# Kernel optimization log

Hardware: AMD Instinct MI355X
Metric: run time of the kernel (lower is better)

Reference implementation:

```python
import jax, jax.numpy as jnp
import numpy as np

B, N, K = 4, 1024, 32
C_S, C_Z, C_H, H, PQ, PV = 384, 128, 16, 12, 4, 8
INF, EPS = 1e5, 1e-8
LN_EPS = 1e-5


def _quat_to_rot(q):
    # q: [..., 4] unit quaternions -> [..., 3, 3]
    w, x, y, z = q[..., 0], q[..., 1], q[..., 2], q[..., 3]
    r = jnp.stack([
        1 - 2 * (y * y + z * z), 2 * (x * y - w * z), 2 * (x * z + w * y),
        2 * (x * y + w * z), 1 - 2 * (x * x + z * z), 2 * (y * z - w * x),
        2 * (x * z - w * y), 2 * (y * z + w * x), 1 - 2 * (x * x + y * y),
    ], axis=-1)
    return r.reshape(q.shape[:-1] + (3, 3))


def _layernorm(x, scale, bias):
    m = jnp.mean(x, axis=-1, keepdims=True)
    v = jnp.mean((x - m) ** 2, axis=-1, keepdims=True)
    return (x - m) * jax.lax.rsqrt(v + LN_EPS) * scale + bias


def setup_inputs():
    key = jax.random.key(0)
    ks = jax.random.split(key, 16)
    s = jax.random.normal(ks[0], (B, N, C_S), jnp.float32)
    z = jax.random.normal(ks[1], (B, N, K, C_Z), jnp.float32)
    edge_index = jax.random.randint(ks[2], (B, N, K), 0, N, jnp.int32)
    quat = jax.random.normal(ks[3], (B, N, 4), jnp.float32)
    rot = _quat_to_rot(quat / jnp.linalg.norm(quat, axis=-1, keepdims=True))
    trans = 10.0 * jax.random.normal(ks[4], (B, N, 3), jnp.float32)
    s_mask = jnp.ones((B, N), jnp.float32)
    sc_s, sc_z = C_S ** -0.5, C_Z ** -0.5
    return {
        "s": s, "z": z, "edge_index": edge_index, "rot": rot, "trans": trans,
        "s_mask": s_mask,
        "ln_s_scale": jnp.ones((C_S,), jnp.float32),
        "ln_s_bias": jnp.zeros((C_S,), jnp.float32),
        "ln_z_scale": jnp.ones((C_Z,), jnp.float32),
        "ln_z_bias": jnp.zeros((C_Z,), jnp.float32),
        "w_q": sc_s * jax.random.normal(ks[5], (C_S, H * C_H), jnp.float32),
        "w_k": sc_s * jax.random.normal(ks[6], (C_S, H * C_H), jnp.float32),
        "w_v": sc_s * jax.random.normal(ks[7], (C_S, H * C_H), jnp.float32),
        "w_q_pts": sc_s * jax.random.normal(ks[8], (C_S, H * PQ * 3), jnp.float32),
        "w_kv_pts": sc_s * jax.random.normal(ks[9], (C_S, H * (PQ + PV) * 3), jnp.float32),
        "w_b": sc_z * jax.random.normal(ks[10], (C_Z, H), jnp.float32),
        "w_down_z": sc_z * jax.random.normal(ks[11], (C_Z, C_Z // 4), jnp.float32),
        "head_weights": jnp.full((H,), 0.541324854612918, jnp.float32),  # softplus^-1(1)
        "w_out": (H * 80) ** -0.5 * jax.random.normal(ks[12], (H * (C_Z // 4 + C_H + PV * 4), C_S), jnp.float32),
    }


def reference(s, z, edge_index, rot, trans, s_mask, ln_s_scale, ln_s_bias,
              ln_z_scale, ln_z_bias, w_q, w_k, w_v, w_q_pts, w_kv_pts, w_b,
              w_down_z, head_weights, w_out):
    bidx = jnp.arange(B)[:, None, None]
    s_ln = _layernorm(s, ln_s_scale, ln_s_bias)          # [B,N,C_S]
    z_ln = _layernorm(z, ln_z_scale, ln_z_bias)          # [B,N,K,C_Z]

    q = (s_ln @ w_q).reshape(B, N, H, C_H)
    k = (s_ln @ w_k)[bidx, edge_index].reshape(B, N, K, H, C_H)
    v = (s_ln @ w_v)[bidx, edge_index].reshape(B, N, K, H, C_H)

    # query points in global frame (query residue's rigid)
    q_pts = (s_ln @ w_q_pts).reshape(B, N, H * PQ, 3)
    q_pts = jnp.einsum('bnij,bnpj->bnpi', rot, q_pts) + trans[:, :, None]
    q_pts = q_pts.reshape(B, N, H, PQ, 3)

    # kv points: gather neighbor local points, then (as in source) apply the
    # QUERY residue's rigid r[..., None, None]
    kv = (s_ln @ w_kv_pts)[bidx, edge_index].reshape(B, N, K, H * (PQ + PV), 3)
    kv = jnp.einsum('bnij,bnkpj->bnkpi', rot, kv) + trans[:, :, None, None]
    kv = kv.reshape(B, N, K, H, PQ + PV, 3)
    k_pts, v_pts = kv[..., :PQ, :], kv[..., PQ:, :]

    b_bias = z_ln @ w_b                                   # [B,N,K,H]
    a = jnp.einsum('bnhc,bnkhc->bnkh', q, k) * (1.0 / (3 * C_H)) ** 0.5
    a = a + (1.0 / 3.0) ** 0.5 * b_bias

    disp = q_pts[:, :, None] - k_pts                      # [B,N,K,H,PQ,3]
    sq = jnp.sum(disp * disp, axis=-1)                    # [B,N,K,H,PQ]
    hw = jax.nn.softplus(head_weights) * (1.0 / (3 * (PQ * 9.0 / 2))) ** 0.5
    a = a - 0.5 * jnp.sum(sq * hw[:, None], axis=-1)      # [B,N,K,H]

    m = s_mask[:, :, None] * s_mask[bidx, edge_index]     # [B,N,K]
    a = a + (INF * (m - 1.0))[..., None]

    a = jax.nn.softmax(jnp.swapaxes(a, -1, -2), axis=-1)  # [B,N,H,K]

    o = jnp.einsum('bnhk,bnkhc->bnhc', a, v).reshape(B, N, H * C_H)

    o_pt = jnp.einsum('bnhk,bnkhvc->bnhvc', a, v_pts)     # [B,N,H,PV,3]
    o_pt = jnp.einsum('bnji,bnhvj->bnhvi', rot, o_pt - trans[:, :, None, None])
    dists = jnp.sqrt(jnp.sum(o_pt * o_pt, axis=-1) + EPS).reshape(B, N, H * PV)
    o_pt_flat = o_pt.reshape(B, N, H * PV * 3)

    o_pair = jnp.einsum('bnhk,bnkc->bnhc', a, z_ln @ w_down_z).reshape(B, N, -1)

    out = jnp.concatenate([o, o_pt_flat, dists, o_pair], axis=-1) @ w_out
    return out
```

## Files before the change

kernel.cpp:

```cpp
#include <hip/hip_runtime.h>
#include <hip/hip_bf16.h>

constexpr int Bb = 4, Nn = 1024, Kk = 32;
constexpr int CS = 384, CZ = 128, CH = 16, Hh = 12, PQn = 4, PVn = 8;
constexpr int HC = Hh * CH;
constexpr int NCOLS = 1152;
constexpr int FEAT = 960;
constexpr int NNODE = Bb * Nn;
constexpr int NEDGE = NNODE * Kk;
constexpr int ZOC = 44;

constexpr int O_WNODE = 4;
constexpr int O_WOUT  = O_WNODE + 384 * 1152;
constexpr int O_WZP   = O_WOUT + 960 * 384;
constexpr int O_BVEC  = O_WZP + 128 * 48;
constexpr int O_SLN   = O_BVEC + 48;
constexpr int O_P     = O_SLN + NNODE * CS;
constexpr int O_ZOUT  = O_P + NNODE * NCOLS;
constexpr int O_FEAT  = O_ZOUT + NEDGE * ZOC;
constexpr int O_MR    = O_FEAT;
constexpr int O_TMP   = O_SLN;
constexpr int TOTAL_F = O_FEAT + NNODE * FEAT;

__device__ __forceinline__ float ldf(const float* p, int i) { return p[i]; }
__device__ __forceinline__ float ldf(const __hip_bfloat16* p, int i) { return __bfloat162float(p[i]); }
__device__ __forceinline__ void stf(float* p, int i, float v) { p[i] = v; }
__device__ __forceinline__ void stf(__hip_bfloat16* p, int i, float v) { p[i] = __float2bfloat16(v); }
__device__ __forceinline__ float4 ld4(const float* p, int i) { return *(const float4*)(p + i); }
__device__ __forceinline__ float4 ld4(const __hip_bfloat16* p, int i) {
    ushort4 u = *(const ushort4*)(p + i);
    return make_float4(__uint_as_float((unsigned)u.x << 16),
                       __uint_as_float((unsigned)u.y << 16),
                       __uint_as_float((unsigned)u.z << 16),
                       __uint_as_float((unsigned)u.w << 16));
}

__global__ void k_detect(const unsigned* smask_raw, int* flag) {
    if (threadIdx.x == 0) *flag = (smask_raw[0] == 0x3F803F80u) ? 1 : 0;
}

template <typename T>
__global__ __launch_bounds__(256) void k_wconv(const T* wq, const T* wk, const T* wv,
                                               const T* wqp, const T* wkvp,
                                               const T* wout, float* wsf,
                                               const int* flag, int want) {
    if (*flag != want) return;
    int idx = blockIdx.x * 256 + threadIdx.x;
    if (idx < 384 * 1152) {
        int row = idx / 1152, col = idx - row * 1152;
        float v;
        if      (col < 192) v = ldf(wq,  row * 192 + col);
        else if (col < 384) v = ldf(wk,  row * 192 + col - 192);
        else if (col < 576) v = ldf(wv,  row * 192 + col - 384);
        else if (col < 720) v = ldf(wqp, row * 144 + col - 576);
        else                v = ldf(wkvp, row * 432 + col - 720);
        wsf[O_WNODE + idx] = v;
    } else if (idx < 384 * 1152 + 960 * 384) {
        int u = idx - 384 * 1152;
        wsf[O_WOUT + u] = ldf(wout, u);
    }
}

template <typename T>
__global__ __launch_bounds__(256) void k_wzprep(const T* wb, const T* wdz, const T* zsc, const T* zbi,
                                                float* wzp, float* bvec, const int* flag, int want) {
    if (*flag != want) return;
    int t = threadIdx.x;
    if (t < 128) {
        float sc = ldf(zsc, t);
        for (int o = 0; o < 48; o++) {
            float w = 0.f;
            if (o < 12)      w = ldf(wb, t * 12 + o);
            else if (o < 44) w = ldf(wdz, t * 32 + o - 12);
            wzp[t * 48 + o] = sc * w;
        }
    } else if (t < 128 + 48) {
        int o = t - 128;
        float acc = 0.f;
        if (o < 44)
            for (int c = 0; c < 128; c++)
                acc += ldf(zbi, c) * (o < 12 ? ldf(wb, c * 12 + o) : ldf(wdz, c * 32 + o - 12));
        bvec[o] = acc;
    }
}

template <typename T>
__global__ __launch_bounds__(384) void k_sln(const T* s, const T* sc, const T* bi,
                                             float* sln, const int* flag, int want) {
    if (*flag != want) return;
    int row = blockIdx.x, t = threadIdx.x;
    float x = ldf(s, row * CS + t);
    float sum = x, sq = x * x;
    #pragma unroll
    for (int m = 32; m; m >>= 1) { sum += __shfl_xor(sum, m, 64); sq += __shfl_xor(sq, m, 64); }
    __shared__ float ssum[6], ssq[6];
    int w = t >> 6;
    if ((t & 63) == 0) { ssum[w] = sum; ssq[w] = sq; }
    __syncthreads();
    if (t == 0) {
        float S = 0, Q = 0;
        for (int i = 0; i < 6; i++) { S += ssum[i]; Q += ssq[i]; }
        ssum[0] = S; ssq[0] = Q;
    }
    __syncthreads();
    float mean = ssum[0] * (1.f / CS);
    float var  = ssq[0] * (1.f / CS) - mean * mean;
    float r = rsqrtf(var + 1e-5f);
    sln[row * CS + t] = (x - mean) * r * ldf(sc, t) + ldf(bi, t);
}

template <typename T>
__global__ __launch_bounds__(256) void k_zstats(const T* z, float* mr, const int* flag, int want) {
    if (*flag != want) return;
    int t = threadIdx.x, r = t >> 5, lane = t & 31;
    int row = blockIdx.x * 8 + r;
    float4 v = ld4(z, row * CZ + lane * 4);
    float sum = v.x + v.y + v.z + v.w;
    float sq  = v.x * v.x + v.y * v.y + v.z * v.z + v.w * v.w;
    #pragma unroll
    for (int m = 16; m; m >>= 1) { sum += __shfl_xor(sum, m, 64); sq += __shfl_xor(sq, m, 64); }
    if (lane == 0) {
        float mean = sum * (1.f / CZ);
        float var  = sq * (1.f / CZ) - mean * mean;
        mr[row * 2]     = mean;
        mr[row * 2 + 1] = rsqrtf(var + 1e-5f);
    }
}

template <typename T>
__global__ __launch_bounds__(256) void k_zgemm(const T* z, const float* mr, const float* wzp,
                                               const float* bvec, float* zout,
                                               const int* flag, int want) {
    if (*flag != want) return;
    __shared__ float Ws[128 * 48];
    __shared__ float As[16][260];
    int t = threadIdx.x;
    int edge0 = blockIdx.x * 256;
    for (int i = t; i < 128 * 48; i += 256) Ws[i] = wzp[i];
    int tm = t >> 2, tn = t & 3, col = tn * 12;
    int sr = t >> 2, q = t & 3;
    float mu[4], rs[4];
    #pragma unroll
    for (int u = 0; u < 4; u++) {
        int e = edge0 + sr + 64 * u;
        mu[u] = mr[e * 2]; rs[u] = mr[e * 2 + 1];
    }
    float acc[4][12];
    #pragma unroll
    for (int i = 0; i < 4; i++)
        #pragma unroll
        for (int j = 0; j < 12; j++) acc[i][j] = bvec[col + j];
    for (int kt = 0; kt < CZ; kt += 16) {
        float4 zv[4];
        #pragma unroll
        for (int u = 0; u < 4; u++) zv[u] = ld4(z, (edge0 + sr + 64 * u) * CZ + kt + q * 4);
        __syncthreads();
        #pragma unroll
        for (int u = 0; u < 4; u++) {
            int rr = sr + 64 * u;
            As[q * 4 + 0][rr] = (zv[u].x - mu[u]) * rs[u];
            As[q * 4 + 1][rr] = (zv[u].y - mu[u]) * rs[u];
            As[q * 4 + 2][rr] = (zv[u].z - mu[u]) * rs[u];
            As[q * 4 + 3][rr] = (zv[u].w - mu[u]) * rs[u];
        }
        __syncthreads();
        #pragma unroll
        for (int kk = 0; kk < 16; kk++) {
            float4 a = *(const float4*)&As[kk][tm * 4];
            const float* wr = &Ws[(kt + kk) * 48 + col];
            float4 b0 = *(const float4*)(wr);
            float4 b1 = *(const float4*)(wr + 4);
            float4 b2 = *(const float4*)(wr + 8);
            float av[4]  = {a.x, a.y, a.z, a.w};
            float bv[12] = {b0.x, b0.y, b0.z, b0.w, b1.x, b1.y, b1.z, b1.w, b2.x, b2.y, b2.z, b2.w};
            #pragma unroll
            for (int i = 0; i < 4; i++)
                #pragma unroll
                for (int j = 0; j < 12; j++) acc[i][j] += av[i] * bv[j];
        }
    }
    #pragma unroll
    for (int i = 0; i < 4; i++) {
        int e = edge0 + tm * 4 + i;
        #pragma unroll
        for (int j = 0; j < 12; j++) {
            int c = col + j;
            if (c < ZOC) zout[e * ZOC + c] = acc[i][j];
        }
    }
}

__global__ __launch_bounds__(256) void k_gemm(const float* A, int lda, const float* Bm, int ldb,
                                              float* C, int ldc, int ksplit, int csplit) {
    __shared__ float As[16][68];
    __shared__ float Bs[16][136];
    int t = threadIdx.x;
    int row0 = blockIdx.x * 64, col0 = blockIdx.y * 128;
    int kbeg = blockIdx.z * ksplit, kend = kbeg + ksplit;
    C += (size_t)blockIdx.z * csplit;
    int tx = t & 15, ty = t >> 4;
    int ar = t >> 2, aq = t & 3;
    int bk = t >> 4, bc = (t & 15) * 8;
    float acc[4][8] = {};
    for (int kt = kbeg; kt < kend; kt += 16) {
        float4 a0 = *(const float4*)(A + (row0 + ar) * lda + kt + aq * 4);
        float4 b0 = *(const float4*)(Bm + (kt + bk) * ldb + col0 + bc);
        float4 b1 = *(const float4*)(Bm + (kt + bk) * ldb + col0 + bc + 4);
        __syncthreads();
        As[aq * 4 + 0][ar] = a0.x; As[aq * 4 + 1][ar] = a0.y;
        As[aq * 4 + 2][ar] = a0.z; As[aq * 4 + 3][ar] = a0.w;
        *(float4*)&Bs[bk][bc] = b0;
        *(float4*)&Bs[bk][bc + 4] = b1;
        __syncthreads();
        #pragma unroll
        for (int kk = 0; kk < 16; kk++) {
            float4 av  = *(const float4*)&As[kk][ty * 4];
            float4 blo = *(const float4*)&Bs[kk][tx * 4];
            float4 bhi = *(const float4*)&Bs[kk][64 + tx * 4];
            float aa[4] = {av.x, av.y, av.z, av.w};
            float bb[8] = {blo.x, blo.y, blo.z, blo.w, bhi.x, bhi.y, bhi.z, bhi.w};
            #pragma unroll
            for (int i = 0; i < 4; i++)
                #pragma unroll
                for (int j = 0; j < 8; j++)
                    acc[i][j] += aa[i] * bb[j];
        }
    }
    #pragma unroll
    for (int i = 0; i < 4; i++) {
        float* Cr = C + (size_t)(row0 + ty * 4 + i) * ldc + col0;
        *(float4*)(Cr + tx * 4)      = make_float4(acc[i][0], acc[i][1], acc[i][2], acc[i][3]);
        *(float4*)(Cr + 64 + tx * 4) = make_float4(acc[i][4], acc[i][5], acc[i][6], acc[i][7]);
    }
}

template <typename TO>
__global__ __launch_bounds__(256) void k_outred(const float* tmp, TO* out, const int* flag, int want) {
    if (*flag != want) return;
    int i = (blockIdx.x * 256 + threadIdx.x) * 4;
    float4 a = *(const float4*)(tmp + i);
    float4 b = *(const float4*)(tmp + NNODE * CS + i);
    stf(out, i,     a.x + b.x); stf(out, i + 1, a.y + b.y);
    stf(out, i + 2, a.z + b.z); stf(out, i + 3, a.w + b.w);
}

template <typename T>
__global__ __launch_bounds__(256, 4) void k_attn(const float* P, const float* zout,
                                                 const int* eidx, const T* smask, const T* rot,
                                                 const T* hwq, float* featg, const int* flag, int want) {
    if (*flag != want) return;
    __shared__ float nds[4][1792];
    __shared__ int js[4][32];
    int w = threadIdx.x >> 6, lane = threadIdx.x & 63;
    int node = blockIdx.x * 4 + w;
    int b = node >> 10;
    float* S = nds[w];
    int* J = js[w];
    const float* Pn = P + (size_t)node * NCOLS;
    for (int u = lane; u < 336; u += 64)
        S[u] = (u < 192) ? Pn[u] : Pn[384 + u];
    if (lane < 32) {
        int j = eidx[node * Kk + lane];
        J[lane] = b * Nn + j;
        S[360 + lane] = ldf(smask, node) * ldf(smask, b * Nn + j);
    } else if (lane < 44) {
        int h = lane - 32;
        float x = ldf(hwq, h);
        S[336 + h] = logf(1.f + expf(x)) * 0.13608276348795434f;
    } else if (lane < 53) {
        int u = lane - 44;
        int i = u / 3, jj = u - i * 3;
        float m = 0;
        #pragma unroll
        for (int l = 0; l < 3; l++)
            m += ldf(rot, node * 9 + l * 3 + i) * ldf(rot, node * 9 + l * 3 + jj);
        S[348 + u] = m;
    }
    __builtin_amdgcn_wave_barrier();
    #pragma unroll
    for (int it = 0; it < 6; it++) {
        int u = lane + 64 * it;
        int h = u >> 5, k = u & 31;
        const float* Pj = P + (size_t)J[k] * NCOLS;
        float qk = 0;
        const float4* pk4 = (const float4*)(Pj + 192 + h * 16);
        const float4* qs4 = (const float4*)(S + h * 16);
        #pragma unroll
        for (int c4 = 0; c4 < 4; c4++) {
            float4 pv = pk4[c4], qv = qs4[c4];
            qk += qv.x * pv.x + qv.y * pv.y + qv.z * pv.z + qv.w * pv.w;
        }
        float M00 = S[348], M01 = S[349], M02 = S[350],
              M11 = S[352], M12 = S[353], M22 = S[356];
        const float4* pp4 = (const float4*)(Pj + 720 + h * 36);
        const float4* qp4 = (const float4*)(S + 192 + h * 12);
        float4 A0 = pp4[0], A1 = pp4[1], A2 = pp4[2];
        float4 B0 = qp4[0], B1 = qp4[1], B2 = qp4[2];
        float d[12] = {B0.x - A0.x, B0.y - A0.y, B0.z - A0.z, B0.w - A0.w,
                       B1.x - A1.x, B1.y - A1.y, B1.z - A1.z, B1.w - A1.w,
                       B2.x - A2.x, B2.y - A2.y, B2.z - A2.z, B2.w - A2.w};
        float sq = 0;
        #pragma unroll
        for (int p = 0; p < 4; p++) {
            float d0 = d[p * 3], d1 = d[p * 3 + 1], d2 = d[p * 3 + 2];
            sq += M00 * d0 * d0 + M11 * d1 * d1 + M22 * d2 * d2
                + 2.f * (M01 * d0 * d1 + M02 * d0 * d2 + M12 * d1 * d2);
        }
        float logit = qk * 0.14433756729740643f
                    + 0.5773502691896258f * zout[((size_t)node * Kk + k) * ZOC + h]
                    - 0.5f * S[336 + h] * sq
                    + 1e5f * (S[360 + k] - 1.f);
        float mx = logit;
        #pragma unroll
        for (int m = 16; m; m >>= 1) mx = fmaxf(mx, __shfl_xor(mx, m, 64));
        float e = expf(logit - mx);
        float ssum = e;
        #pragma unroll
        for (int m = 16; m; m >>= 1) ssum += __shfl_xor(ssum, m, 64);
        S[392 + u] = e / ssum;
    }
    __builtin_amdgcn_wave_barrier();
    for (int u = lane; u < 216; u += 64) {
        int h, off, fbase, pair = 0;
        if (u < 48)       { h = u >> 2; off = 384 + h * 16 + (u & 3) * 4; fbase = h * 16 + (u & 3) * 4; }
        else if (u < 120) { int v = u - 48;  h = v / 6; int q = v - h * 6;
                            off = 732 + h * 36 + q * 4; fbase = 192 + h * 24 + q * 4; }
        else              { int v = u - 120; h = v >> 3;
                            off = 12 + (v & 7) * 4; fbase = 576 + h * 32 + (v & 7) * 4; pair = 1; }
        float4 acc = {0.f, 0.f, 0.f, 0.f};
        const float* lrow = S + 392 + h * 32;
        if (!pair) {
            #pragma unroll 8
            for (int k = 0; k < 32; k++) {
                float lw = lrow[k];
                float4 pv = *(const float4*)(P + (size_t)J[k] * NCOLS + off);
                acc.x += lw * pv.x; acc.y += lw * pv.y; acc.z += lw * pv.z; acc.w += lw * pv.w;
            }
        } else {
            const float* zr = zout + (size_t)node * Kk * ZOC + off;
            #pragma unroll 8
            for (int k = 0; k < 32; k++) {
                float lw = lrow[k];
                float4 pv = *(const float4*)(zr + k * ZOC);
                acc.x += lw * pv.x; acc.y += lw * pv.y; acc.z += lw * pv.z; acc.w += lw * pv.w;
            }
        }
        *(float4*)&S[776 + fbase] = acc;
    }
    __builtin_amdgcn_wave_barrier();
    for (int u = lane; u < 96; u += 64) {
        float r0 = S[776 + 192 + u * 3 + 0];
        float r1 = S[776 + 192 + u * 3 + 1];
        float r2 = S[776 + 192 + u * 3 + 2];
        float o0 = S[348] * r0 + S[349] * r1 + S[350] * r2;
        float o1 = S[351] * r0 + S[352] * r1 + S[353] * r2;
        float o2 = S[354] * r0 + S[355] * r1 + S[356] * r2;
        S[776 + 192 + u * 3 + 0] = o0;
        S[776 + 192 + u * 3 + 1] = o1;
        S[776 + 192 + u * 3 + 2] = o2;
        S[776 + 480 + u] = sqrtf(o0 * o0 + o1 * o1 + o2 * o2 + 1e-8f);
    }
    __builtin_amdgcn_wave_barrier();
    float* og = featg + (size_t)node * FEAT;
    for (int u = lane; u < 240; u += 64)
        *(float4*)(og + u * 4) = *(const float4*)&S[776 + u * 4];
}

extern "C" void kernel_launch(void* const* d_in, const int* in_sizes, int n_in,
                              void* d_out, int out_size, void* d_ws, size_t ws_size,
                              hipStream_t stream) {
    float* wsf = (float*)d_ws;
    int* flag = (int*)d_ws;
    const void* s = d_in[0];   const void* z = d_in[1];
    const int* eidx = (const int*)d_in[2];
    const void* rot = d_in[3];
    const void* smask = d_in[5];
    const void* lns_sc = d_in[6]; const void* lns_bi = d_in[7];
    const void* lnz_sc = d_in[8]; const void* lnz_bi = d_in[9];
    const void* wq = d_in[10]; const void* wk = d_in[11]; const void* wv = d_in[12];
    const void* wqp = d_in[13]; const void* wkvp = d_in[14];
    const void* wb = d_in[15]; const void* wdz = d_in[16];
    const void* hwq = d_in[17]; const void* wout = d_in[18];

    k_detect<<<1, 64, 0, stream>>>((const unsigned*)smask, flag);

    constexpr int WCONV_N = (384 * 1152 + 960 * 384) / 256;
    k_wconv<float><<<WCONV_N, 256, 0, stream>>>((const float*)wq, (const float*)wk, (const float*)wv,
        (const float*)wqp, (const float*)wkvp, (const float*)wout, wsf, flag, 0);
    k_wconv<__hip_bfloat16><<<WCONV_N, 256, 0, stream>>>((const __hip_bfloat16*)wq,
        (const __hip_bfloat16*)wk, (const __hip_bfloat16*)wv, (const __hip_bfloat16*)wqp,
        (const __hip_bfloat16*)wkvp, (const __hip_bfloat16*)wout, wsf, flag, 1);

    k_wzprep<float><<<1, 256, 0, stream>>>((const float*)wb, (const float*)wdz,
        (const float*)lnz_sc, (const float*)lnz_bi, wsf + O_WZP, wsf + O_BVEC, flag, 0);
    k_wzprep<__hip_bfloat16><<<1, 256, 0, stream>>>((const __hip_bfloat16*)wb, (const __hip_bfloat16*)wdz,
        (const __hip_bfloat16*)lnz_sc, (const __hip_bfloat16*)lnz_bi, wsf + O_WZP, wsf + O_BVEC, flag, 1);

    k_sln<float><<<NNODE, 384, 0, stream>>>((const float*)s, (const float*)lns_sc, (const float*)lns_bi,
                                            wsf + O_SLN, flag, 0);
    k_sln<__hip_bfloat16><<<NNODE, 384, 0, stream>>>((const __hip_bfloat16*)s, (const __hip_bfloat16*)lns_sc,
                                                     (const __hip_bfloat16*)lns_bi, wsf + O_SLN, flag, 1);

    k_zstats<float><<<NEDGE / 8, 256, 0, stream>>>((const float*)z, wsf + O_MR, flag, 0);
    k_zstats<__hip_bfloat16><<<NEDGE / 8, 256, 0, stream>>>((const __hip_bfloat16*)z, wsf + O_MR, flag, 1);

    k_zgemm<float><<<NEDGE / 256, 256, 0, stream>>>((const float*)z, wsf + O_MR, wsf + O_WZP,
        wsf + O_BVEC, wsf + O_ZOUT, flag, 0);
    k_zgemm<__hip_bfloat16><<<NEDGE / 256, 256, 0, stream>>>((const __hip_bfloat16*)z, wsf + O_MR,
        wsf + O_WZP, wsf + O_BVEC, wsf + O_ZOUT, flag, 1);

    k_gemm<<<dim3(NNODE / 64, NCOLS / 128, 1), 256, 0, stream>>>(
        wsf + O_SLN, CS, wsf + O_WNODE, NCOLS, wsf + O_P, NCOLS, CS, 0);

    k_attn<float><<<NNODE / 4, 256, 0, stream>>>(wsf + O_P, wsf + O_ZOUT, eidx,
        (const float*)smask, (const float*)rot, (const float*)hwq, wsf + O_FEAT, flag, 0);
    k_attn<__hip_bfloat16><<<NNODE / 4, 256, 0, stream>>>(wsf + O_P, wsf + O_ZOUT, eidx,
        (const float*)smask == nullptr ? (const __hip_bfloat16*)smask : (const __hip_bfloat16*)smask,
        (const __hip_bfloat16*)rot, (const __hip_bfloat16*)hwq, wsf + O_FEAT, flag, 1);

    k_gemm<<<dim3(NNODE / 64, CS / 128, 2), 256, 0, stream>>>(
        wsf + O_FEAT, FEAT, wsf + O_WOUT, CS, wsf + O_TMP, CS, FEAT / 2, NNODE * CS);
    k_outred<float><<<NNODE * CS / 1024, 256, 0, stream>>>(wsf + O_TMP, (float*)d_out, flag, 0);
    k_outred<__hip_bfloat16><<<NNODE * CS / 1024, 256, 0, stream>>>(wsf + O_TMP,
        (__hip_bfloat16*)d_out, flag, 1);
}
```

Measured before the change: 389.0 us.

## Fuse prep kernels, fold z layernorm into GEMM epilogue, drop split-K output

Merges weight conversion, s-layernorm and z-weight prep into one launch, and folds the z layernorm statistics into the z GEMM by applying mean and rstd algebraically in the epilogue through a column-sum vector. The split-K output GEMM plus reduction kernel is replaced by a single smaller-tile GEMM that writes the output directly. Host-side dtype detection from input sizes skips the detect kernel and the duplicate dtype-guarded launches. The attention kernel also gets a swizzled block-to-node mapping, a padded softmax row stride and a dropped occupancy hint. Computing variance from E[x^2]-mean^2 on raw z can lose precision, and the output GEMM has less parallelism without split-K.

```diff
diff --git a/kernel.cpp b/kernel.cpp
--- a/kernel.cpp
+++ b/kernel.cpp
@@ -14,12 +14,11 @@
 constexpr int O_WOUT  = O_WNODE + 384 * 1152;
 constexpr int O_WZP   = O_WOUT + 960 * 384;
 constexpr int O_BVEC  = O_WZP + 128 * 48;
-constexpr int O_SLN   = O_BVEC + 48;
+constexpr int O_CSUM  = O_BVEC + 48;
+constexpr int O_SLN   = O_CSUM + 48;
 constexpr int O_P     = O_SLN + NNODE * CS;
 constexpr int O_ZOUT  = O_P + NNODE * NCOLS;
 constexpr int O_FEAT  = O_ZOUT + NEDGE * ZOC;
-constexpr int O_MR    = O_FEAT;
-constexpr int O_TMP   = O_SLN;
 constexpr int TOTAL_F = O_FEAT + NNODE * FEAT;
 
 __device__ __forceinline__ float ldf(const float* p, int i) { return p[i]; }
@@ -40,128 +39,107 @@
 }
 
 template <typename T>
-__global__ __launch_bounds__(256) void k_wconv(const T* wq, const T* wk, const T* wv,
-                                               const T* wqp, const T* wkvp,
-                                               const T* wout, float* wsf,
-                                               const int* flag, int want) {
-    if (*flag != want) return;
-    int idx = blockIdx.x * 256 + threadIdx.x;
-    if (idx < 384 * 1152) {
-        int row = idx / 1152, col = idx - row * 1152;
-        float v;
-        if      (col < 192) v = ldf(wq,  row * 192 + col);
-        else if (col < 384) v = ldf(wk,  row * 192 + col - 192);
-        else if (col < 576) v = ldf(wv,  row * 192 + col - 384);
-        else if (col < 720) v = ldf(wqp, row * 144 + col - 576);
-        else                v = ldf(wkvp, row * 432 + col - 720);
-        wsf[O_WNODE + idx] = v;
-    } else if (idx < 384 * 1152 + 960 * 384) {
-        int u = idx - 384 * 1152;
-        wsf[O_WOUT + u] = ldf(wout, u);
+__global__ __launch_bounds__(384) void k_prep(const T* s, const T* lns_sc, const T* lns_bi,
+                                              const T* wq, const T* wk, const T* wv,
+                                              const T* wqp, const T* wkvp, const T* wout,
+                                              const T* wb, const T* wdz, const T* zsc, const T* zbi,
+                                              float* wsf, const int* flag, int want) {
+    if (flag && *flag != want) return;
+    int blk = blockIdx.x, t = threadIdx.x;
+    __shared__ float ssum[6], ssq[6];
+    if (blk < 2112) {
+        int idx = blk * 384 + t;
+        if (idx < 384 * 1152) {
+            int row = idx / 1152, col = idx - row * 1152;
+            float v;
+            if      (col < 192) v = ldf(wq,  row * 192 + col);
+            else if (col < 384) v = ldf(wk,  row * 192 + col - 192);
+            else if (col < 576) v = ldf(wv,  row * 192 + col - 384);
+            else if (col < 720) v = ldf(wqp, row * 144 + col - 576);
+            else                v = ldf(wkvp, row * 432 + col - 720);
+            wsf[O_WNODE + idx] = v;
+        } else {
+            int u = idx - 384 * 1152;
+            wsf[O_WOUT + u] = ldf(wout, u);
+        }
+    } else if (blk < 2112 + 4096) {
+        int row = blk - 2112;
+        float x = ldf(s, row * CS + t);
+        float sum = x, sq = x * x;
+        #pragma unroll
+        for (int m = 32; m; m >>= 1) { sum += __shfl_xor(sum, m, 64); sq += __shfl_xor(sq, m, 64); }
+        int w = t >> 6;
+        if ((t & 63) == 0) { ssum[w] = sum; ssq[w] = sq; }
+        __syncthreads();
+        if (t == 0) {
+            float S = 0, Q = 0;
+            for (int i = 0; i < 6; i++) { S += ssum[i]; Q += ssq[i]; }
+            ssum[0] = S; ssq[0] = Q;
+        }
+        __syncthreads();
+        float mean = ssum[0] * (1.f / CS);
+        float var  = ssq[0] * (1.f / CS) - mean * mean;
+        float r = rsqrtf(var + 1e-5f);
+        wsf[O_SLN + row * CS + t] = (x - mean) * r * ldf(lns_sc, t) + ldf(lns_bi, t);
+    } else {
+        if (t < 128) {
+            float sc = ldf(zsc, t);
+            for (int o = 0; o < 48; o++) {
+                float w = 0.f;
+                if (o < 12)      w = ldf(wb, t * 12 + o);
+                else if (o < 44) w = ldf(wdz, t * 32 + o - 12);
+                wsf[O_WZP + t * 48 + o] = sc * w;
+            }
+        } else if (t < 176) {
+            int o = t - 128;
+            float acc = 0.f;
+            if (o < 44)
+                for (int c = 0; c < 128; c++)
+                    acc += ldf(zbi, c) * (o < 12 ? ldf(wb, c * 12 + o) : ldf(wdz, c * 32 + o - 12));
+            wsf[O_BVEC + o] = acc;
+        } else if (t < 224) {
+            int o = t - 176;
+            float acc = 0.f;
+            if (o < 44)
+                for (int c = 0; c < 128; c++)
+                    acc += ldf(zsc, c) * (o < 12 ? ldf(wb, c * 12 + o) : ldf(wdz, c * 32 + o - 12));
+            wsf[O_CSUM + o] = acc;
+        }
     }
 }
 
 template <typename T>
-__global__ __launch_bounds__(256) void k_wzprep(const T* wb, const T* wdz, const T* zsc, const T* zbi,
-                                                float* wzp, float* bvec, const int* flag, int want) {
-    if (*flag != want) return;
-    int t = threadIdx.x;
-    if (t < 128) {
-        float sc = ldf(zsc, t);
-        for (int o = 0; o < 48; o++) {
-            float w = 0.f;
-            if (o < 12)      w = ldf(wb, t * 12 + o);
-            else if (o < 44) w = ldf(wdz, t * 32 + o - 12);
-            wzp[t * 48 + o] = sc * w;
-        }
-    } else if (t < 128 + 48) {
-        int o = t - 128;
-        float acc = 0.f;
-        if (o < 44)
-            for (int c = 0; c < 128; c++)
-                acc += ldf(zbi, c) * (o < 12 ? ldf(wb, c * 12 + o) : ldf(wdz, c * 32 + o - 12));
-        bvec[o] = acc;
-    }
-}
-
-template <typename T>
-__global__ __launch_bounds__(384) void k_sln(const T* s, const T* sc, const T* bi,
-                                             float* sln, const int* flag, int want) {
-    if (*flag != want) return;
-    int row = blockIdx.x, t = threadIdx.x;
-    float x = ldf(s, row * CS + t);
-    float sum = x, sq = x * x;
-    #pragma unroll
-    for (int m = 32; m; m >>= 1) { sum += __shfl_xor(sum, m, 64); sq += __shfl_xor(sq, m, 64); }
-    __shared__ float ssum[6], ssq[6];
-    int w = t >> 6;
-    if ((t & 63) == 0) { ssum[w] = sum; ssq[w] = sq; }
-    __syncthreads();
-    if (t == 0) {
-        float S = 0, Q = 0;
-        for (int i = 0; i < 6; i++) { S += ssum[i]; Q += ssq[i]; }
-        ssum[0] = S; ssq[0] = Q;
-    }
-    __syncthreads();
-    float mean = ssum[0] * (1.f / CS);
-    float var  = ssq[0] * (1.f / CS) - mean * mean;
-    float r = rsqrtf(var + 1e-5f);
-    sln[row * CS + t] = (x - mean) * r * ldf(sc, t) + ldf(bi, t);
-}
-
-template <typename T>
-__global__ __launch_bounds__(256) void k_zstats(const T* z, float* mr, const int* flag, int want) {
-    if (*flag != want) return;
-    int t = threadIdx.x, r = t >> 5, lane = t & 31;
-    int row = blockIdx.x * 8 + r;
-    float4 v = ld4(z, row * CZ + lane * 4);
-    float sum = v.x + v.y + v.z + v.w;
-    float sq  = v.x * v.x + v.y * v.y + v.z * v.z + v.w * v.w;
-    #pragma unroll
-    for (int m = 16; m; m >>= 1) { sum += __shfl_xor(sum, m, 64); sq += __shfl_xor(sq, m, 64); }
-    if (lane == 0) {
-        float mean = sum * (1.f / CZ);
-        float var  = sq * (1.f / CZ) - mean * mean;
-        mr[row * 2]     = mean;
-        mr[row * 2 + 1] = rsqrtf(var + 1e-5f);
-    }
-}
-
-template <typename T>
-__global__ __launch_bounds__(256) void k_zgemm(const T* z, const float* mr, const float* wzp,
-                                               const float* bvec, float* zout,
-                                               const int* flag, int want) {
-    if (*flag != want) return;
+__global__ __launch_bounds__(256) void k_zg(const T* z, const float* wzp, const float* bvec,
+                                            const float* csum, float* zout,
+                                            const int* flag, int want) {
+    if (flag && *flag != want) return;
     __shared__ float Ws[128 * 48];
     __shared__ float As[16][260];
+    __shared__ float mus[256], rss[256];
     int t = threadIdx.x;
     int edge0 = blockIdx.x * 256;
     for (int i = t; i < 128 * 48; i += 256) Ws[i] = wzp[i];
     int tm = t >> 2, tn = t & 3, col = tn * 12;
     int sr = t >> 2, q = t & 3;
-    float mu[4], rs[4];
-    #pragma unroll
-    for (int u = 0; u < 4; u++) {
-        int e = edge0 + sr + 64 * u;
-        mu[u] = mr[e * 2]; rs[u] = mr[e * 2 + 1];
-    }
-    float acc[4][12];
-    #pragma unroll
-    for (int i = 0; i < 4; i++)
-        #pragma unroll
-        for (int j = 0; j < 12; j++) acc[i][j] = bvec[col + j];
+    float psum[4] = {}, psq[4] = {};
+    float acc[4][12] = {};
     for (int kt = 0; kt < CZ; kt += 16) {
         float4 zv[4];
         #pragma unroll
-        for (int u = 0; u < 4; u++) zv[u] = ld4(z, (edge0 + sr + 64 * u) * CZ + kt + q * 4);
+        for (int u = 0; u < 4; u++) {
+            zv[u] = ld4(z, (edge0 + sr + 64 * u) * CZ + kt + q * 4);
+            psum[u] += zv[u].x + zv[u].y + zv[u].z + zv[u].w;
+            psq[u]  += zv[u].x * zv[u].x + zv[u].y * zv[u].y
+                     + zv[u].z * zv[u].z + zv[u].w * zv[u].w;
+        }
         __syncthreads();
         #pragma unroll
         for (int u = 0; u < 4; u++) {
             int rr = sr + 64 * u;
-            As[q * 4 + 0][rr] = (zv[u].x - mu[u]) * rs[u];
-            As[q * 4 + 1][rr] = (zv[u].y - mu[u]) * rs[u];
-            As[q * 4 + 2][rr] = (zv[u].z - mu[u]) * rs[u];
-            As[q * 4 + 3][rr] = (zv[u].w - mu[u]) * rs[u];
+            As[q * 4 + 0][rr] = zv[u].x;
+            As[q * 4 + 1][rr] = zv[u].y;
+            As[q * 4 + 2][rr] = zv[u].z;
+            As[q * 4 + 3][rr] = zv[u].w;
         }
         __syncthreads();
         #pragma unroll
@@ -178,34 +156,47 @@
                 #pragma unroll
                 for (int j = 0; j < 12; j++) acc[i][j] += av[i] * bv[j];
         }
-    }
+        __syncthreads();
+    }
+    #pragma unroll
+    for (int u = 0; u < 4; u++) {
+        float s = psum[u], qq = psq[u];
+        s += __shfl_xor(s, 1, 64); s += __shfl_xor(s, 2, 64);
+        qq += __shfl_xor(qq, 1, 64); qq += __shfl_xor(qq, 2, 64);
+        if (q == 0) {
+            float mu = s * (1.f / CZ);
+            mus[sr + 64 * u] = mu;
+            rss[sr + 64 * u] = rsqrtf(qq * (1.f / CZ) - mu * mu + 1e-5f);
+        }
+    }
+    __syncthreads();
     #pragma unroll
     for (int i = 0; i < 4; i++) {
-        int e = edge0 + tm * 4 + i;
+        int r = tm * 4 + i;
+        float mu = mus[r], rs = rss[r];
+        int e = edge0 + r;
         #pragma unroll
         for (int j = 0; j < 12; j++) {
             int c = col + j;
-            if (c < ZOC) zout[e * ZOC + c] = acc[i][j];
+            if (c < ZOC) zout[(size_t)e * ZOC + c] = rs * acc[i][j] - rs * mu * csum[c] + bvec[c];
         }
     }
 }
 
 __global__ __launch_bounds__(256) void k_gemm(const float* A, int lda, const float* Bm, int ldb,
-                                              float* C, int ldc, int ksplit, int csplit) {
+                                              float* C, int ldc, int Kdim) {
     __shared__ float As[16][68];
     __shared__ float Bs[16][136];
     int t = threadIdx.x;
     int row0 = blockIdx.x * 64, col0 = blockIdx.y * 128;
-    int kbeg = blockIdx.z * ksplit, kend = kbeg + ksplit;
-    C += (size_t)blockIdx.z * csplit;
     int tx = t & 15, ty = t >> 4;
     int ar = t >> 2, aq = t & 3;
     int bk = t >> 4, bc = (t & 15) * 8;
     float acc[4][8] = {};
-    for (int kt = kbeg; kt < kend; kt += 16) {
-        float4 a0 = *(const float4*)(A + (row0 + ar) * lda + kt + aq * 4);
-        float4 b0 = *(const float4*)(Bm + (kt + bk) * ldb + col0 + bc);
-        float4 b1 = *(const float4*)(Bm + (kt + bk) * ldb + col0 + bc + 4);
+    for (int kt = 0; kt < Kdim; kt += 16) {
+        float4 a0 = *(const float4*)(A + (size_t)(row0 + ar) * lda + kt + aq * 4);
+        float4 b0 = *(const float4*)(Bm + (size_t)(kt + bk) * ldb + col0 + bc);
+        float4 b1 = *(const float4*)(Bm + (size_t)(kt + bk) * ldb + col0 + bc + 4);
         __syncthreads();
         As[aq * 4 + 0][ar] = a0.x; As[aq * 4 + 1][ar] = a0.y;
         As[aq * 4 + 2][ar] = a0.z; As[aq * 4 + 3][ar] = a0.w;
@@ -235,24 +226,56 @@
 }
 
 template <typename TO>
-__global__ __launch_bounds__(256) void k_outred(const float* tmp, TO* out, const int* flag, int want) {
-    if (*flag != want) return;
-    int i = (blockIdx.x * 256 + threadIdx.x) * 4;
-    float4 a = *(const float4*)(tmp + i);
-    float4 b = *(const float4*)(tmp + NNODE * CS + i);
-    stf(out, i,     a.x + b.x); stf(out, i + 1, a.y + b.y);
-    stf(out, i + 2, a.z + b.z); stf(out, i + 3, a.w + b.w);
+__global__ __launch_bounds__(256) void k_gout(const float* A, const float* Bm, TO* C,
+                                              const int* flag, int want) {
+    if (flag && *flag != want) return;
+    __shared__ float As[16][36];
+    __shared__ float Bs[16][68];
+    int t = threadIdx.x;
+    int row0 = blockIdx.x * 32, col0 = blockIdx.y * 64;
+    int ar = (t >> 2) & 31, aq = t & 3;
+    int bk = t >> 4, bc = (t & 15) * 4;
+    int ty = t >> 4, tx = t & 15;
+    int m0 = ty * 2, n0 = tx * 4;
+    float acc[2][4] = {};
+    for (int kt = 0; kt < FEAT; kt += 16) {
+        float4 av = {};
+        if (t < 128) av = *(const float4*)(A + (size_t)(row0 + ar) * FEAT + kt + aq * 4);
+        float4 bv = *(const float4*)(Bm + (size_t)(kt + bk) * CS + col0 + bc);
+        __syncthreads();
+        if (t < 128) {
+            As[aq * 4 + 0][ar] = av.x; As[aq * 4 + 1][ar] = av.y;
+            As[aq * 4 + 2][ar] = av.z; As[aq * 4 + 3][ar] = av.w;
+        }
+        *(float4*)&Bs[bk][bc] = bv;
+        __syncthreads();
+        #pragma unroll
+        for (int kk = 0; kk < 16; kk++) {
+            float a0 = As[kk][m0], a1 = As[kk][m0 + 1];
+            float4 b = *(const float4*)&Bs[kk][n0];
+            acc[0][0] += a0 * b.x; acc[0][1] += a0 * b.y; acc[0][2] += a0 * b.z; acc[0][3] += a0 * b.w;
+            acc[1][0] += a1 * b.x; acc[1][1] += a1 * b.y; acc[1][2] += a1 * b.z; acc[1][3] += a1 * b.w;
+        }
+        __syncthreads();
+    }
+    #pragma unroll
+    for (int i = 0; i < 2; i++)
+        #pragma unroll
+        for (int j = 0; j < 4; j++)
+            stf(C, (size_t)(row0 + m0 + i) * CS + col0 + n0 + j, acc[i][j]);
 }
 
 template <typename T>
-__global__ __launch_bounds__(256, 4) void k_attn(const float* P, const float* zout,
-                                                 const int* eidx, const T* smask, const T* rot,
-                                                 const T* hwq, float* featg, const int* flag, int want) {
-    if (*flag != want) return;
-    __shared__ float nds[4][1792];
+__global__ __launch_bounds__(256) void k_attn(const float* P, const float* zout,
+                                              const int* eidx, const T* smask, const T* rot,
+                                              const T* hwq, float* featg, const int* flag, int want) {
+    if (flag && *flag != want) return;
+    __shared__ float nds[4][1760];
     __shared__ int js[4][32];
+    int bid = blockIdx.x;
+    int nb = ((bid & 7) << 7) + (bid >> 3);
     int w = threadIdx.x >> 6, lane = threadIdx.x & 63;
-    int node = blockIdx.x * 4 + w;
+    int node = nb * 4 + w;
     int b = node >> 10;
     float* S = nds[w];
     int* J = js[w];
@@ -317,7 +340,7 @@
         float ssum = e;
         #pragma unroll
         for (int m = 16; m; m >>= 1) ssum += __shfl_xor(ssum, m, 64);
-        S[392 + u] = e / ssum;
+        S[392 + h * 33 + k] = e / ssum;
     }
     __builtin_amdgcn_wave_barrier();
     for (int u = lane; u < 216; u += 64) {
@@ -328,7 +351,7 @@
         else              { int v = u - 120; h = v >> 3;
                             off = 12 + (v & 7) * 4; fbase = 576 + h * 32 + (v & 7) * 4; pair = 1; }
         float4 acc = {0.f, 0.f, 0.f, 0.f};
-        const float* lrow = S + 392 + h * 32;
+        const float* lrow = S + 392 + h * 33;
         if (!pair) {
             #pragma unroll 8
             for (int k = 0; k < 32; k++) {
@@ -345,25 +368,25 @@
                 acc.x += lw * pv.x; acc.y += lw * pv.y; acc.z += lw * pv.z; acc.w += lw * pv.w;
             }
         }
-        *(float4*)&S[776 + fbase] = acc;
+        *(float4*)&S[788 + fbase] = acc;
     }
     __builtin_amdgcn_wave_barrier();
     for (int u = lane; u < 96; u += 64) {
-        float r0 = S[776 + 192 + u * 3 + 0];
-        float r1 = S[776 + 192 + u * 3 + 1];
-        float r2 = S[776 + 192 + u * 3 + 2];
+        float r0 = S[788 + 192 + u * 3 + 0];
+        float r1 = S[788 + 192 + u * 3 + 1];
+        float r2 = S[788 + 192 + u * 3 + 2];
         float o0 = S[348] * r0 + S[349] * r1 + S[350] * r2;
         float o1 = S[351] * r0 + S[352] * r1 + S[353] * r2;
         float o2 = S[354] * r0 + S[355] * r1 + S[356] * r2;
-        S[776 + 192 + u * 3 + 0] = o0;
-        S[776 + 192 + u * 3 + 1] = o1;
-        S[776 + 192 + u * 3 + 2] = o2;
-        S[776 + 480 + u] = sqrtf(o0 * o0 + o1 * o1 + o2 * o2 + 1e-8f);
+        S[788 + 192 + u * 3 + 0] = o0;
+        S[788 + 192 + u * 3 + 1] = o1;
+        S[788 + 192 + u * 3 + 2] = o2;
+        S[788 + 480 + u] = sqrtf(o0 * o0 + o1 * o1 + o2 * o2 + 1e-8f);
     }
     __builtin_amdgcn_wave_barrier();
     float* og = featg + (size_t)node * FEAT;
     for (int u = lane; u < 240; u += 64)
-        *(float4*)(og + u * 4) = *(const float4*)&S[776 + u * 4];
+        *(float4*)(og + u * 4) = *(const float4*)&S[788 + u * 4];
 }
 
 extern "C" void kernel_launch(void* const* d_in, const int* in_sizes, int n_in,
@@ -382,45 +405,57 @@
     const void* wb = d_in[15]; const void* wdz = d_in[16];
     const void* hwq = d_in[17]; const void* wout = d_in[18];
 
-    k_detect<<<1, 64, 0, stream>>>((const unsigned*)smask, flag);
-
-    constexpr int WCONV_N = (384 * 1152 + 960 * 384) / 256;
-    k_wconv<float><<<WCONV_N, 256, 0, stream>>>((const float*)wq, (const float*)wk, (const float*)wv,
-        (const float*)wqp, (const float*)wkvp, (const float*)wout, wsf, flag, 0);
-    k_wconv<__hip_bfloat16><<<WCONV_N, 256, 0, stream>>>((const __hip_bfloat16*)wq,
-        (const __hip_bfloat16*)wk, (const __hip_bfloat16*)wv, (const __hip_bfloat16*)wqp,
-        (const __hip_bfloat16*)wkvp, (const __hip_bfloat16*)wout, wsf, flag, 1);
-
-    k_wzprep<float><<<1, 256, 0, stream>>>((const float*)wb, (const float*)wdz,
-        (const float*)lnz_sc, (const float*)lnz_bi, wsf + O_WZP, wsf + O_BVEC, flag, 0);
-    k_wzprep<__hip_bfloat16><<<1, 256, 0, stream>>>((const __hip_bfloat16*)wb, (const __hip_bfloat16*)wdz,
-        (const __hip_bfloat16*)lnz_sc, (const __hip_bfloat16*)lnz_bi, wsf + O_WZP, wsf + O_BVEC, flag, 1);
-
-    k_sln<float><<<NNODE, 384, 0, stream>>>((const float*)s, (const float*)lns_sc, (const float*)lns_bi,
-                                            wsf + O_SLN, flag, 0);
-    k_sln<__hip_bfloat16><<<NNODE, 384, 0, stream>>>((const __hip_bfloat16*)s, (const __hip_bfloat16*)lns_sc,
-                                                     (const __hip_bfloat16*)lns_bi, wsf + O_SLN, flag, 1);
-
-    k_zstats<float><<<NEDGE / 8, 256, 0, stream>>>((const float*)z, wsf + O_MR, flag, 0);
-    k_zstats<__hip_bfloat16><<<NEDGE / 8, 256, 0, stream>>>((const __hip_bfloat16*)z, wsf + O_MR, flag, 1);
-
-    k_zgemm<float><<<NEDGE / 256, 256, 0, stream>>>((const float*)z, wsf + O_MR, wsf + O_WZP,
-        wsf + O_BVEC, wsf + O_ZOUT, flag, 0);
-    k_zgemm<__hip_bfloat16><<<NEDGE / 256, 256, 0, stream>>>((const __hip_bfloat16*)z, wsf + O_MR,
-        wsf + O_WZP, wsf + O_BVEC, wsf + O_ZOUT, flag, 1);
-
-    k_gemm<<<dim3(NNODE / 64, NCOLS / 128, 1), 256, 0, stream>>>(
-        wsf + O_SLN, CS, wsf + O_WNODE, NCOLS, wsf + O_P, NCOLS, CS, 0);
-
-    k_attn<float><<<NNODE / 4, 256, 0, stream>>>(wsf + O_P, wsf + O_ZOUT, eidx,
-        (const float*)smask, (const float*)rot, (const float*)hwq, wsf + O_FEAT, flag, 0);
-    k_attn<__hip_bfloat16><<<NNODE / 4, 256, 0, stream>>>(wsf + O_P, wsf + O_ZOUT, eidx,
-        (const float*)smask == nullptr ? (const __hip_bfloat16*)smask : (const __hip_bfloat16*)smask,
-        (const __hip_bfloat16*)rot, (const __hip_bfloat16*)hwq, wsf + O_FEAT, flag, 1);
-
-    k_gemm<<<dim3(NNODE / 64, CS / 128, 2), 256, 0, stream>>>(
-        wsf + O_FEAT, FEAT, wsf + O_WOUT, CS, wsf + O_TMP, CS, FEAT / 2, NNODE * CS);
-    k_outred<float><<<NNODE * CS / 1024, 256, 0, stream>>>(wsf + O_TMP, (float*)d_out, flag, 0);
-    k_outred<__hip_bfloat16><<<NNODE * CS / 1024, 256, 0, stream>>>(wsf + O_TMP,
-        (__hip_bfloat16*)d_out, flag, 1);
-}
+    int mode = -1;
+    if (in_sizes) {
+        if (in_sizes[0] == NNODE * CS * 4) mode = 0;
+        else if (in_sizes[0] == NNODE * CS * 2) mode = 1;
+    }
+
+    const int* fg = (mode < 0) ? flag : nullptr;
+    if (mode < 0) k_detect<<<1, 64, 0, stream>>>((const unsigned*)smask, flag);
+
+    #define LAUNCH_T(T, WANT)                                                                     \
+        do {                                                                                      \
+            k_prep<T><<<2112 + 4096 + 1, 384, 0, stream>>>((const T*)s, (const T*)lns_sc,         \
+                (const T*)lns_bi, (const T*)wq, (const T*)wk, (const T*)wv, (const T*)wqp,        \
+                (const T*)wkvp, (const T*)wout, (const T*)wb, (const T*)wdz, (const T*)lnz_sc,    \
+                (const T*)lnz_bi, wsf, fg, WANT);                                                 \
+            k_zg<T><<<NEDGE / 256, 256, 0, stream>>>((const T*)z, wsf + O_WZP, wsf + O_BVEC,      \
+                wsf + O_CSUM, wsf + O_ZOUT, fg, WANT);                                            \
+        } while (0)
+
+    #define LAUNCH_ATTN(T, WANT)                                                                  \
+        k_attn<T><<<NNODE / 4, 256, 0, stream>>>(wsf + O_P, wsf + O_ZOUT, eidx,                   \
+            (const T*)smask, (const T*)rot, (const T*)hwq, wsf + O_FEAT, fg, WANT)
+
+    if (mode == 0) {
+        LAUNCH_T(float, 0);
+    } else if (mode == 1) {
+        LAUNCH_T(__hip_bfloat16, 1);
+    } else {
+        LAUNCH_T(float, 0);
+        LAUNCH_T(__hip_bfloat16, 1);
+    }
+
+    k_gemm<<<dim3(NNODE / 64, NCOLS / 128), 256, 0, stream>>>(
+        wsf + O_SLN, CS, wsf + O_WNODE, NCOLS, wsf + O_P, NCOLS, CS);
+
+    if (mode == 0) {
+        LAUNCH_ATTN(float, 0);
+        k_gout<float><<<dim3(NNODE / 32, CS / 64), 256, 0, stream>>>(
+            wsf + O_FEAT, wsf + O_WOUT, (float*)d_out, fg, 0);
+    } else if (mode == 1) {
+        LAUNCH_ATTN(__hip_bfloat16, 1);
+        k_gout<__hip_bfloat16><<<dim3(NNODE / 32, CS / 64), 256, 0, stream>>>(
+            wsf + O_FEAT, wsf + O_WOUT, (__hip_bfloat16*)d_out, fg, 1);
+    } else {
+        LAUNCH_ATTN(float, 0);
+        LAUNCH_ATTN(__hip_bfloat16, 1);
+        k_gout<float><<<dim3(NNODE / 32, CS / 64), 256, 0, stream>>>(
+            wsf + O_FEAT, wsf + O_WOUT, (float*)d_out, fg, 0);
+        k_gout<__hip_bfloat16><<<dim3(NNODE / 32, CS / 64), 256, 0, stream>>>(
+            wsf + O_FEAT, wsf + O_WOUT, (__hip_bfloat16*)d_out, fg, 1);
+    }
+    #undef LAUNCH_T
+    #undef LAUNCH_ATTN
+}
```

Result: faster. 376.7 us (-3.2%).
